# Kernel optimization log

Hardware: AMD Instinct MI355X
Metric: run time of the kernel (lower is better)

## Reference

```python
import jax, jax.numpy as jnp
import numpy as np
from jax import lax

DUNITS = 1024
ATT_DIM = 512
EPROJS = 512
ACONV_CHANS = 10
ACONV_FILTS = 100  # kernel size = 2*100+1 = 201
H_LEN = 16384
N_PREV = 128
SCALING = 2.0


def setup_inputs() -> dict:
    key = jax.random.key(0)
    ks = jax.random.split(key, 10)
    inv = lambda fan_in: 1.0 / np.sqrt(fan_in)
    return {
        "dec_z": jax.random.normal(ks[0], (1, DUNITS), jnp.float32),
        "att_prev": jax.random.uniform(ks[1], (N_PREV, 1, H_LEN), jnp.float32) / H_LEN,
        "pre_compute_enc_h": jax.random.normal(ks[2], (1, H_LEN, ATT_DIM), jnp.float32),
        "enc_h": jax.random.normal(ks[3], (1, H_LEN, EPROJS), jnp.float32),
        "mask": jnp.zeros((1, H_LEN), jnp.float32),
        # parameters (torch default inits, scale by 1/sqrt(fan_in))
        "loc_conv_w": jax.random.normal(ks[4], (ACONV_CHANS, 1, 2 * ACONV_FILTS + 1), jnp.float32) * inv(2 * ACONV_FILTS + 1),
        "mlp_att_w": jax.random.normal(ks[5], (ATT_DIM, ACONV_CHANS), jnp.float32) * inv(ACONV_CHANS),
        "mlp_dec_w": jax.random.normal(ks[6], (ATT_DIM, DUNITS), jnp.float32) * inv(DUNITS),
        "gvec_w": jax.random.normal(ks[7], (1, ATT_DIM), jnp.float32) * inv(ATT_DIM),
        "gvec_b": jnp.zeros((1,), jnp.float32),
    }


def reference(dec_z, att_prev, pre_compute_enc_h, enc_h, mask,
              loc_conv_w, mlp_att_w, mlp_dec_w, gvec_w, gvec_b):
    h_length = enc_h.shape[1]
    dec_z = dec_z.reshape(1, DUNITS)

    # coverage vector: sum of all previous attention distributions -> [1, h]
    cov_vec = jnp.sum(att_prev, axis=0)

    # location conv: Conv2d(1, C, (1, 2F+1)) on [1,1,1,h] == 1D conv on [1,1,h]
    att_conv = lax.conv_general_dilated(
        cov_vec[:, None, :], loc_conv_w,
        window_strides=(1,), padding=[(ACONV_FILTS, ACONV_FILTS)],
        dimension_numbers=("NCH", "OIH", "NCH"),
    )  # [1, C, h]
    # squeeze/transpose then mlp_att (no bias): [1, h, att_dim]
    att_conv = jnp.einsum("bch,ac->bha", att_conv, mlp_att_w)

    # mlp_dec (no bias), tiled over h: [1, 1, att_dim]
    dec_z_tiled = (dec_z @ mlp_dec_w.T)[:, None, :]

    # additive attention score e: [1, h]
    t = jnp.tanh(att_conv + pre_compute_enc_h + dec_z_tiled)
    e = jnp.einsum("bha,oa->bho", t, gvec_w)[..., 0] + gvec_b
    e = e + mask

    w = jax.nn.softmax(SCALING * e, axis=1)  # [1, h]

    att_prev_new = jnp.concatenate([att_prev, w[None]], axis=0)  # [n+1, 1, h]
    c = jnp.sum(enc_h * w[:, :, None], axis=1)  # [1, eprojs]
    return (c, att_prev_new)
```

## Files before the change

### kernel.cpp

```cpp
#include <hip/hip_runtime.h>

#define H_LEN 16384
#define ATT_DIM 512
#define DUNITS 1024
#define EPROJS 512
#define NCH 10
#define KFILT 201
#define PAD 100
#define N_PREV 128
#define HB 32
#define NB_SCORE 512
#define NB_FIN 256
#define NCOVP 16

__global__ __launch_bounds__(256) void k_prep(const float* __restrict__ att_prev,
                                              const float* __restrict__ mlp_dec_w,
                                              const float* __restrict__ dec_z,
                                              const float* __restrict__ watt,
                                              float* __restrict__ out_prev,
                                              float* __restrict__ cov16,
                                              float* __restrict__ dz,
                                              float* __restrict__ wattT,
                                              float* __restrict__ out_c) {
    int b = blockIdx.x, tid = threadIdx.x;
    if (b < 256) {
        const float4* ap4 = (const float4*)att_prev;
        float4* op4 = (float4*)out_prev;
        float4* cv4 = (float4*)cov16;
        int hb = b >> 4, q = b & 15;
        int idx0 = hb * 256 + tid;
        float4 s = {0.f, 0.f, 0.f, 0.f};
        #pragma unroll
        for (int n = q * 8; n < q * 8 + 8; ++n) {
            float4 v = ap4[n * (H_LEN / 4) + idx0];
            s.x += v.x; s.y += v.y; s.z += v.z; s.w += v.w;
            op4[n * (H_LEN / 4) + idx0] = v;
        }
        cv4[q * (H_LEN / 4) + idx0] = s;
    } else if (b < 384) {
        int lane = tid & 63;
        int a = (b - 256) * 4 + (tid >> 6);
        const float* row = mlp_dec_w + a * DUNITS;
        float s = 0.f;
        #pragma unroll
        for (int t = 0; t < DUNITS / 64; ++t) s += row[lane + 64 * t] * dec_z[lane + 64 * t];
        #pragma unroll
        for (int off = 32; off > 0; off >>= 1) s += __shfl_xor(s, off, 64);
        if (lane == 0) dz[a] = s;
    } else {
        out_c[tid] = 0.f;
        out_c[tid + 256] = 0.f;
        int a = tid * 2;
        #pragma unroll
        for (int c = 0; c < NCH; ++c) {
            wattT[c * ATT_DIM + a]     = watt[a * NCH + c];
            wattT[c * ATT_DIM + a + 1] = watt[(a + 1) * NCH + c];
        }
    }
}

__global__ __launch_bounds__(256, 2) void k_score(const float* __restrict__ cov16,
                                                  const float* __restrict__ cw,
                                                  const float* __restrict__ pre,
                                                  const float* __restrict__ mask,
                                                  const float* __restrict__ dz,
                                                  const float* __restrict__ wattT,
                                                  const float* __restrict__ gv,
                                                  const float* __restrict__ gb,
                                                  const float* __restrict__ enc,
                                                  float* __restrict__ vbuf,
                                                  float* __restrict__ pm,
                                                  float* __restrict__ ps,
                                                  float* __restrict__ pcb) {
    __shared__ float cov_s[HB + 2 * PAD];
    __shared__ float mask_s[HB];
    __shared__ float pc[8][NCH][HB];
    __shared__ float cfT[HB * 12];
    __shared__ float ew[4][HB];
    __shared__ float wt[HB];

    int tid = threadIdx.x, b = blockIdx.x;
    int h0 = b * HB;
    int lane = tid & 63, wv = tid >> 6;

    for (int i = tid; i < HB + 2 * PAD; i += 256) {
        int g = h0 - PAD + i;
        float s = 0.f;
        if (g >= 0 && g < H_LEN) {
            #pragma unroll
            for (int q = 0; q < NCOVP; ++q) s += cov16[q * H_LEN + g];
        }
        cov_s[i] = s;
    }
    if (tid < HB) mask_s[tid] = mask[h0 + tid];

    int a = (wv << 7) + (lane << 1);
    float2 dz2 = *(const float2*)(dz + a);
    float2 gv2 = *(const float2*)(gv + a);
    float W0[NCH], W1[NCH];
    #pragma unroll
    for (int c = 0; c < NCH; ++c) {
        float2 w = *(const float2*)(wattT + c * ATT_DIM + a);
        W0[c] = w.x; W1[c] = w.y;
    }
    float bias = gb[0];
    __syncthreads();

    {
        int h = tid & 31, q = tid >> 5;
        int k0 = (q * KFILT) / 8, k1 = ((q + 1) * KFILT) / 8;
        float acc[NCH];
        #pragma unroll
        for (int c = 0; c < NCH; ++c) acc[c] = 0.f;
        for (int k = k0; k < k1; ++k) {
            float s = cov_s[h + k];
            #pragma unroll
            for (int c = 0; c < NCH; ++c) acc[c] += s * cw[c * KFILT + k];
        }
        #pragma unroll
        for (int c = 0; c < NCH; ++c) pc[q][c][h] = acc[c];
    }
    __syncthreads();
    for (int i = tid; i < NCH * HB; i += 256) {
        int c = i >> 5, h = i & 31;
        float s = 0.f;
        #pragma unroll
        for (int q = 0; q < 8; ++q) s += pc[q][c][h];
        cfT[h * 12 + c] = s;
    }
    __syncthreads();

    float ea[HB];
    const float2* pre2 = (const float2*)pre;
    int colf2 = (wv << 6) + lane;
    #pragma unroll
    for (int hc = 0; hc < HB; hc += 8) {
        float2 Pr[8];
        #pragma unroll
        for (int j = 0; j < 8; ++j) Pr[j] = pre2[(h0 + hc + j) * 256 + colf2];
        #pragma unroll
        for (int j = 0; j < 8; ++j) {
            int h = hc + j;
            const float4* cp = (const float4*)&cfT[h * 12];
            float4 c0 = cp[0], c1 = cp[1], c2 = cp[2];
            float ch[NCH] = {c0.x, c0.y, c0.z, c0.w, c1.x, c1.y, c1.z, c1.w, c2.x, c2.y};
            float x0 = Pr[j].x + dz2.x;
            float x1 = Pr[j].y + dz2.y;
            #pragma unroll
            for (int c = 0; c < NCH; ++c) { x0 += ch[c] * W0[c]; x1 += ch[c] * W1[c]; }
            x0 = fminf(fmaxf(x0, -15.f), 15.f);
            x1 = fminf(fmaxf(x1, -15.f), 15.f);
            float z0 = __expf(2.f * x0), z1 = __expf(2.f * x1);
            float t0 = (z0 - 1.f) * __builtin_amdgcn_rcpf(z0 + 1.f);
            float t1 = (z1 - 1.f) * __builtin_amdgcn_rcpf(z1 + 1.f);
            ea[h] = t0 * gv2.x + t1 * gv2.y;
        }
    }

    #pragma unroll
    for (int k = 0; k < 16; ++k) {
        float up = __shfl_xor(ea[k + 16], 32, 64);
        float dn = __shfl_xor(ea[k], 32, 64);
        ea[k] = (lane & 32) ? (ea[k + 16] + up) : (ea[k] + dn);
    }
    #pragma unroll
    for (int k = 0; k < 8; ++k) {
        float up = __shfl_xor(ea[k + 8], 16, 64);
        float dn = __shfl_xor(ea[k], 16, 64);
        ea[k] = (lane & 16) ? (ea[k + 8] + up) : (ea[k] + dn);
    }
    #pragma unroll
    for (int k = 0; k < 4; ++k) {
        float up = __shfl_xor(ea[k + 4], 8, 64);
        float dn = __shfl_xor(ea[k], 8, 64);
        ea[k] = (lane & 8) ? (ea[k + 4] + up) : (ea[k] + dn);
    }
    #pragma unroll
    for (int k = 0; k < 2; ++k) {
        float up = __shfl_xor(ea[k + 2], 4, 64);
        float dn = __shfl_xor(ea[k], 4, 64);
        ea[k] = (lane & 4) ? (ea[k + 2] + up) : (ea[k] + dn);
    }
    {
        float up = __shfl_xor(ea[1], 2, 64);
        float dn = __shfl_xor(ea[0], 2, 64);
        ea[0] = (lane & 2) ? (ea[1] + up) : (ea[0] + dn);
    }
    ea[0] += __shfl_xor(ea[0], 1, 64);
    if ((lane & 1) == 0) ew[wv][lane >> 1] = ea[0];
    __syncthreads();

    if (wv == 0) {
        float v = -1e30f;
        if (lane < HB) {
            float e = ew[0][lane] + ew[1][lane] + ew[2][lane] + ew[3][lane];
            v = 2.f * (e + bias + mask_s[lane]);
            vbuf[h0 + lane] = v;
        }
        float m = v;
        #pragma unroll
        for (int off = 32; off > 0; off >>= 1) m = fmaxf(m, __shfl_xor(m, off, 64));
        float ev = (lane < HB) ? __expf(v - m) : 0.f;
        if (lane < HB) wt[lane] = ev;
        float s = ev;
        #pragma unroll
        for (int off = 32; off > 0; off >>= 1) s += __shfl_xor(s, off, 64);
        if (lane == 0) { pm[b] = m; ps[b] = s; }
    }
    __syncthreads();

    const float2* enc2 = (const float2*)enc;
    float2 acc0 = {0.f, 0.f}, acc1 = {0.f, 0.f};
    #pragma unroll
    for (int h = 0; h < HB; h += 2) {
        float w0 = wt[h], w1 = wt[h + 1];
        float2 e0 = enc2[(h0 + h) * 256 + tid];
        float2 e1 = enc2[(h0 + h + 1) * 256 + tid];
        acc0.x += w0 * e0.x; acc0.y += w0 * e0.y;
        acc1.x += w1 * e1.x; acc1.y += w1 * e1.y;
    }
    float2 accv = {acc0.x + acc1.x, acc0.y + acc1.y};
    ((float2*)pcb)[b * 256 + tid] = accv;
}

__global__ __launch_bounds__(256) void k_final(const float* __restrict__ vbuf,
                                               const float* __restrict__ pm,
                                               const float* __restrict__ ps,
                                               const float* __restrict__ pcb,
                                               float* __restrict__ out_w,
                                               float* __restrict__ out_c) {
    __shared__ float redA[4], redB[4];
    int tid = threadIdx.x, b = blockIdx.x;
    int lane = tid & 63, wv = tid >> 6;

    float m0 = pm[tid], m1 = pm[tid + 256];
    float s0 = ps[tid], s1 = ps[tid + 256];
    float m = fmaxf(m0, m1);
    #pragma unroll
    for (int off = 32; off > 0; off >>= 1) m = fmaxf(m, __shfl_xor(m, off, 64));
    if (lane == 0) redA[wv] = m;
    __syncthreads();
    float M = fmaxf(fmaxf(redA[0], redA[1]), fmaxf(redA[2], redA[3]));
    float s = s0 * __expf(m0 - M) + s1 * __expf(m1 - M);
    #pragma unroll
    for (int off = 32; off > 0; off >>= 1) s += __shfl_xor(s, off, 64);
    if (lane == 0) redB[wv] = s;
    __syncthreads();
    float S = redB[0] + redB[1] + redB[2] + redB[3];
    float rinv = 1.f / S;

    if (tid < 64) {
        int h = b * 64 + tid;
        out_w[h] = __expf(vbuf[h] - M) * rinv;
    }

    int r0 = 2 * b, r1 = 2 * b + 1;
    float sc0 = __expf(pm[r0] - M) * rinv;
    float sc1 = __expf(pm[r1] - M) * rinv;
    float v0 = pcb[r0 * EPROJS + tid] * sc0 + pcb[r1 * EPROJS + tid] * sc1;
    float v1 = pcb[r0 * EPROJS + tid + 256] * sc0 + pcb[r1 * EPROJS + tid + 256] * sc1;
    atomicAdd(&out_c[tid], v0);
    atomicAdd(&out_c[tid + 256], v1);
}

extern "C" void kernel_launch(void* const* d_in, const int* in_sizes, int n_in,
                              void* d_out, int out_size, void* d_ws, size_t ws_size,
                              hipStream_t stream) {
    const float* dec_z      = (const float*)d_in[0];
    const float* att_prev   = (const float*)d_in[1];
    const float* pre        = (const float*)d_in[2];
    const float* enc_h      = (const float*)d_in[3];
    const float* mask       = (const float*)d_in[4];
    const float* loc_conv_w = (const float*)d_in[5];
    const float* mlp_att_w  = (const float*)d_in[6];
    const float* mlp_dec_w  = (const float*)d_in[7];
    const float* gvec_w     = (const float*)d_in[8];
    const float* gvec_b     = (const float*)d_in[9];

    float* out_c    = (float*)d_out;
    float* out_prev = out_c + EPROJS;
    float* out_w    = out_prev + N_PREV * H_LEN;

    float* ws    = (float*)d_ws;
    float* cov16 = ws;
    float* dz    = cov16 + NCOVP * H_LEN;
    float* vb    = dz + ATT_DIM;
    float* pm    = vb + H_LEN;
    float* ps    = pm + NB_SCORE;
    float* pcb   = ps + NB_SCORE;
    float* wattT = pcb + NB_SCORE * EPROJS;

    k_prep<<<385, 256, 0, stream>>>(att_prev, mlp_dec_w, dec_z, mlp_att_w,
                                    out_prev, cov16, dz, wattT, out_c);
    k_score<<<NB_SCORE, 256, 0, stream>>>(cov16, loc_conv_w, pre, mask, dz, wattT,
                                          gvec_w, gvec_b, enc_h, vb, pm, ps, pcb);
    k_final<<<NB_FIN, 256, 0, stream>>>(vb, pm, ps, pcb, out_w, out_c);
}
```

Baseline: 139.2 us.

## Widen score kernel to 512 threads with one attention column per thread

The score kernel now runs 512 threads per block, each handling one attention/encoder column instead of two, with float2 loads replaced by scalar loads. The location-conv partial sums are split 16 ways and the score reduction runs across 8 waves. The butterfly shuffle reduction is rewritten to send a single value per stage instead of two. This aims to raise occupancy and latency hiding for the memory-bound pass, at the cost of narrower loads, more LDS partials and more cross-wave reduction.

```diff
diff --git a/kernel.cpp b/kernel.cpp
--- a/kernel.cpp
+++ b/kernel.cpp
@@ -59,7 +59,7 @@
     }
 }
 
-__global__ __launch_bounds__(256, 2) void k_score(const float* __restrict__ cov16,
+__global__ __launch_bounds__(512, 4) void k_score(const float* __restrict__ cov16,
                                                   const float* __restrict__ cw,
                                                   const float* __restrict__ pre,
                                                   const float* __restrict__ mask,
@@ -74,16 +74,16 @@
                                                   float* __restrict__ pcb) {
     __shared__ float cov_s[HB + 2 * PAD];
     __shared__ float mask_s[HB];
-    __shared__ float pc[8][NCH][HB];
+    __shared__ float pc[16][NCH][HB];
     __shared__ float cfT[HB * 12];
-    __shared__ float ew[4][HB];
+    __shared__ float ew[8][HB];
     __shared__ float wt[HB];
 
     int tid = threadIdx.x, b = blockIdx.x;
     int h0 = b * HB;
     int lane = tid & 63, wv = tid >> 6;
 
-    for (int i = tid; i < HB + 2 * PAD; i += 256) {
+    for (int i = tid; i < HB + 2 * PAD; i += 512) {
         int g = h0 - PAD + i;
         float s = 0.f;
         if (g >= 0 && g < H_LEN) {
@@ -94,21 +94,18 @@
     }
     if (tid < HB) mask_s[tid] = mask[h0 + tid];
 
-    int a = (wv << 7) + (lane << 1);
-    float2 dz2 = *(const float2*)(dz + a);
-    float2 gv2 = *(const float2*)(gv + a);
-    float W0[NCH], W1[NCH];
-    #pragma unroll
-    for (int c = 0; c < NCH; ++c) {
-        float2 w = *(const float2*)(wattT + c * ATT_DIM + a);
-        W0[c] = w.x; W1[c] = w.y;
-    }
+    int a = (wv << 6) + lane;
+    float dz1 = dz[a];
+    float gv1 = gv[a];
+    float W[NCH];
+    #pragma unroll
+    for (int c = 0; c < NCH; ++c) W[c] = wattT[c * ATT_DIM + a];
     float bias = gb[0];
     __syncthreads();
 
     {
         int h = tid & 31, q = tid >> 5;
-        int k0 = (q * KFILT) / 8, k1 = ((q + 1) * KFILT) / 8;
+        int k0 = (q * KFILT) / 16, k1 = ((q + 1) * KFILT) / 16;
         float acc[NCH];
         #pragma unroll
         for (int c = 0; c < NCH; ++c) acc[c] = 0.f;
@@ -121,70 +118,70 @@
         for (int c = 0; c < NCH; ++c) pc[q][c][h] = acc[c];
     }
     __syncthreads();
-    for (int i = tid; i < NCH * HB; i += 256) {
+    for (int i = tid; i < NCH * HB; i += 512) {
         int c = i >> 5, h = i & 31;
         float s = 0.f;
         #pragma unroll
-        for (int q = 0; q < 8; ++q) s += pc[q][c][h];
+        for (int q = 0; q < 16; ++q) s += pc[q][c][h];
         cfT[h * 12 + c] = s;
     }
     __syncthreads();
 
     float ea[HB];
-    const float2* pre2 = (const float2*)pre;
-    int colf2 = (wv << 6) + lane;
     #pragma unroll
     for (int hc = 0; hc < HB; hc += 8) {
-        float2 Pr[8];
-        #pragma unroll
-        for (int j = 0; j < 8; ++j) Pr[j] = pre2[(h0 + hc + j) * 256 + colf2];
+        float Pr[8];
+        #pragma unroll
+        for (int j = 0; j < 8; ++j) Pr[j] = pre[(h0 + hc + j) * ATT_DIM + a];
         #pragma unroll
         for (int j = 0; j < 8; ++j) {
             int h = hc + j;
             const float4* cp = (const float4*)&cfT[h * 12];
             float4 c0 = cp[0], c1 = cp[1], c2 = cp[2];
             float ch[NCH] = {c0.x, c0.y, c0.z, c0.w, c1.x, c1.y, c1.z, c1.w, c2.x, c2.y};
-            float x0 = Pr[j].x + dz2.x;
-            float x1 = Pr[j].y + dz2.y;
-            #pragma unroll
-            for (int c = 0; c < NCH; ++c) { x0 += ch[c] * W0[c]; x1 += ch[c] * W1[c]; }
-            x0 = fminf(fmaxf(x0, -15.f), 15.f);
-            x1 = fminf(fmaxf(x1, -15.f), 15.f);
-            float z0 = __expf(2.f * x0), z1 = __expf(2.f * x1);
-            float t0 = (z0 - 1.f) * __builtin_amdgcn_rcpf(z0 + 1.f);
-            float t1 = (z1 - 1.f) * __builtin_amdgcn_rcpf(z1 + 1.f);
-            ea[h] = t0 * gv2.x + t1 * gv2.y;
+            float x = Pr[j] + dz1;
+            #pragma unroll
+            for (int c = 0; c < NCH; ++c) x += ch[c] * W[c];
+            x = fminf(fmaxf(x, -15.f), 15.f);
+            float z = __expf(2.f * x);
+            float t = (z - 1.f) * __builtin_amdgcn_rcpf(z + 1.f);
+            ea[h] = t * gv1;
         }
     }
 
     #pragma unroll
     for (int k = 0; k < 16; ++k) {
-        float up = __shfl_xor(ea[k + 16], 32, 64);
-        float dn = __shfl_xor(ea[k], 32, 64);
-        ea[k] = (lane & 32) ? (ea[k + 16] + up) : (ea[k] + dn);
+        float lo = ea[k], hi = ea[k + 16];
+        float send = (lane & 32) ? lo : hi;
+        float recv = __shfl_xor(send, 32, 64);
+        ea[k] = ((lane & 32) ? hi : lo) + recv;
     }
     #pragma unroll
     for (int k = 0; k < 8; ++k) {
-        float up = __shfl_xor(ea[k + 8], 16, 64);
-        float dn = __shfl_xor(ea[k], 16, 64);
-        ea[k] = (lane & 16) ? (ea[k + 8] + up) : (ea[k] + dn);
+        float lo = ea[k], hi = ea[k + 8];
+        float send = (lane & 16) ? lo : hi;
+        float recv = __shfl_xor(send, 16, 64);
+        ea[k] = ((lane & 16) ? hi : lo) + recv;
     }
     #pragma unroll
     for (int k = 0; k < 4; ++k) {
-        float up = __shfl_xor(ea[k + 4], 8, 64);
-        float dn = __shfl_xor(ea[k], 8, 64);
-        ea[k] = (lane & 8) ? (ea[k + 4] + up) : (ea[k] + dn);
+        float lo = ea[k], hi = ea[k + 4];
+        float send = (lane & 8) ? lo : hi;
+        float recv = __shfl_xor(send, 8, 64);
+        ea[k] = ((lane & 8) ? hi : lo) + recv;
     }
     #pragma unroll
     for (int k = 0; k < 2; ++k) {
-        float up = __shfl_xor(ea[k + 2], 4, 64);
-        float dn = __shfl_xor(ea[k], 4, 64);
-        ea[k] = (lane & 4) ? (ea[k + 2] + up) : (ea[k] + dn);
+        float lo = ea[k], hi = ea[k + 2];
+        float send = (lane & 4) ? lo : hi;
+        float recv = __shfl_xor(send, 4, 64);
+        ea[k] = ((lane & 4) ? hi : lo) + recv;
     }
     {
-        float up = __shfl_xor(ea[1], 2, 64);
-        float dn = __shfl_xor(ea[0], 2, 64);
-        ea[0] = (lane & 2) ? (ea[1] + up) : (ea[0] + dn);
+        float lo = ea[0], hi = ea[1];
+        float send = (lane & 2) ? lo : hi;
+        float recv = __shfl_xor(send, 2, 64);
+        ea[0] = ((lane & 2) ? hi : lo) + recv;
     }
     ea[0] += __shfl_xor(ea[0], 1, 64);
     if ((lane & 1) == 0) ew[wv][lane >> 1] = ea[0];
@@ -193,7 +190,9 @@
     if (wv == 0) {
         float v = -1e30f;
         if (lane < HB) {
-            float e = ew[0][lane] + ew[1][lane] + ew[2][lane] + ew[3][lane];
+            float e = 0.f;
+            #pragma unroll
+            for (int w = 0; w < 8; ++w) e += ew[w][lane];
             v = 2.f * (e + bias + mask_s[lane]);
             vbuf[h0 + lane] = v;
         }
@@ -209,18 +208,13 @@
     }
     __syncthreads();
 
-    const float2* enc2 = (const float2*)enc;
-    float2 acc0 = {0.f, 0.f}, acc1 = {0.f, 0.f};
+    float ca0 = 0.f, ca1 = 0.f;
     #pragma unroll
     for (int h = 0; h < HB; h += 2) {
-        float w0 = wt[h], w1 = wt[h + 1];
-        float2 e0 = enc2[(h0 + h) * 256 + tid];
-        float2 e1 = enc2[(h0 + h + 1) * 256 + tid];
-        acc0.x += w0 * e0.x; acc0.y += w0 * e0.y;
-        acc1.x += w1 * e1.x; acc1.y += w1 * e1.y;
-    }
-    float2 accv = {acc0.x + acc1.x, acc0.y + acc1.y};
-    ((float2*)pcb)[b * 256 + tid] = accv;
+        ca0 += wt[h]     * enc[(h0 + h) * EPROJS + tid];
+        ca1 += wt[h + 1] * enc[(h0 + h + 1) * EPROJS + tid];
+    }
+    pcb[b * EPROJS + tid] = ca0 + ca1;
 }
 
 __global__ __launch_bounds__(256) void k_final(const float* __restrict__ vbuf,
@@ -292,7 +286,7 @@
 
     k_prep<<<385, 256, 0, stream>>>(att_prev, mlp_dec_w, dec_z, mlp_att_w,
                                     out_prev, cov16, dz, wattT, out_c);
-    k_score<<<NB_SCORE, 256, 0, stream>>>(cov16, loc_conv_w, pre, mask, dz, wattT,
+    k_score<<<NB_SCORE, 512, 0, stream>>>(cov16, loc_conv_w, pre, mask, dz, wattT,
                                           gvec_w, gvec_b, enc_h, vb, pm, ps, pcb);
     k_final<<<NB_FIN, 256, 0, stream>>>(vb, pm, ps, pcb, out_w, out_c);
 }
```

Result: slower. 145.9 us (+4.8%).

## Move att_prev copy into score kernel and halve shuffles in transpose-reduce

Applied to the files above, without the earlier changes.

The 8 MB copy of att_prev into the output is taken out of the prep kernel, which now only reads att_prev to build the coverage partials, and placed at the tail of each score block. Each of the 512 blocks copies 16 KB, so the copy shares the kernel with the compute-heavy scoring work, and prep becomes a read-only pass. The butterfly transpose-reduction now picks the value to send before the shuffle, so each stage issues one shuffle instead of two. The risk is that the score kernel carries extra memory traffic and register pressure, and att_prev is read twice from memory.

```diff
diff --git a/kernel.cpp b/kernel.cpp
--- a/kernel.cpp
+++ b/kernel.cpp
@@ -17,7 +17,6 @@
                                               const float* __restrict__ mlp_dec_w,
                                               const float* __restrict__ dec_z,
                                               const float* __restrict__ watt,
-                                              float* __restrict__ out_prev,
                                               float* __restrict__ cov16,
                                               float* __restrict__ dz,
                                               float* __restrict__ wattT,
@@ -25,7 +24,6 @@
     int b = blockIdx.x, tid = threadIdx.x;
     if (b < 256) {
         const float4* ap4 = (const float4*)att_prev;
-        float4* op4 = (float4*)out_prev;
         float4* cv4 = (float4*)cov16;
         int hb = b >> 4, q = b & 15;
         int idx0 = hb * 256 + tid;
@@ -34,7 +32,6 @@
         for (int n = q * 8; n < q * 8 + 8; ++n) {
             float4 v = ap4[n * (H_LEN / 4) + idx0];
             s.x += v.x; s.y += v.y; s.z += v.z; s.w += v.w;
-            op4[n * (H_LEN / 4) + idx0] = v;
         }
         cv4[q * (H_LEN / 4) + idx0] = s;
     } else if (b < 384) {
@@ -68,6 +65,8 @@
                                                   const float* __restrict__ gv,
                                                   const float* __restrict__ gb,
                                                   const float* __restrict__ enc,
+                                                  const float* __restrict__ att_prev,
+                                                  float* __restrict__ out_prev,
                                                   float* __restrict__ vbuf,
                                                   float* __restrict__ pm,
                                                   float* __restrict__ ps,
@@ -159,32 +158,37 @@
 
     #pragma unroll
     for (int k = 0; k < 16; ++k) {
-        float up = __shfl_xor(ea[k + 16], 32, 64);
-        float dn = __shfl_xor(ea[k], 32, 64);
-        ea[k] = (lane & 32) ? (ea[k + 16] + up) : (ea[k] + dn);
+        float lo = ea[k], hi = ea[k + 16];
+        float send = (lane & 32) ? lo : hi;
+        float recv = __shfl_xor(send, 32, 64);
+        ea[k] = ((lane & 32) ? hi : lo) + recv;
     }
     #pragma unroll
     for (int k = 0; k < 8; ++k) {
-        float up = __shfl_xor(ea[k + 8], 16, 64);
-        float dn = __shfl_xor(ea[k], 16, 64);
-        ea[k] = (lane & 16) ? (ea[k + 8] + up) : (ea[k] + dn);
+        float lo = ea[k], hi = ea[k + 8];
+        float send = (lane & 16) ? lo : hi;
+        float recv = __shfl_xor(send, 16, 64);
+        ea[k] = ((lane & 16) ? hi : lo) + recv;
     }
     #pragma unroll
     for (int k = 0; k < 4; ++k) {
-        float up = __shfl_xor(ea[k + 4], 8, 64);
-        float dn = __shfl_xor(ea[k], 8, 64);
-        ea[k] = (lane & 8) ? (ea[k + 4] + up) : (ea[k] + dn);
+        float lo = ea[k], hi = ea[k + 4];
+        float send = (lane & 8) ? lo : hi;
+        float recv = __shfl_xor(send, 8, 64);
+        ea[k] = ((lane & 8) ? hi : lo) + recv;
     }
     #pragma unroll
     for (int k = 0; k < 2; ++k) {
-        float up = __shfl_xor(ea[k + 2], 4, 64);
-        float dn = __shfl_xor(ea[k], 4, 64);
-        ea[k] = (lane & 4) ? (ea[k + 2] + up) : (ea[k] + dn);
+        float lo = ea[k], hi = ea[k + 2];
+        float send = (lane & 4) ? lo : hi;
+        float recv = __shfl_xor(send, 4, 64);
+        ea[k] = ((lane & 4) ? hi : lo) + recv;
     }
     {
-        float up = __shfl_xor(ea[1], 2, 64);
-        float dn = __shfl_xor(ea[0], 2, 64);
-        ea[0] = (lane & 2) ? (ea[1] + up) : (ea[0] + dn);
+        float lo = ea[0], hi = ea[1];
+        float send = (lane & 2) ? lo : hi;
+        float recv = __shfl_xor(send, 2, 64);
+        ea[0] = ((lane & 2) ? hi : lo) + recv;
     }
     ea[0] += __shfl_xor(ea[0], 1, 64);
     if ((lane & 1) == 0) ew[wv][lane >> 1] = ea[0];
@@ -221,6 +225,14 @@
     }
     float2 accv = {acc0.x + acc1.x, acc0.y + acc1.y};
     ((float2*)pcb)[b * 256 + tid] = accv;
+
+    {
+        const float4* ap4 = (const float4*)att_prev;
+        float4* op4 = (float4*)out_prev;
+        int ci = b * 1024 + tid;
+        #pragma unroll
+        for (int r = 0; r < 4; ++r) op4[ci + 256 * r] = ap4[ci + 256 * r];
+    }
 }
 
 __global__ __launch_bounds__(256) void k_final(const float* __restrict__ vbuf,
@@ -291,8 +303,9 @@
     float* wattT = pcb + NB_SCORE * EPROJS;
 
     k_prep<<<385, 256, 0, stream>>>(att_prev, mlp_dec_w, dec_z, mlp_att_w,
-                                    out_prev, cov16, dz, wattT, out_c);
+                                    cov16, dz, wattT, out_c);
     k_score<<<NB_SCORE, 256, 0, stream>>>(cov16, loc_conv_w, pre, mask, dz, wattT,
-                                          gvec_w, gvec_b, enc_h, vb, pm, ps, pcb);
+                                          gvec_w, gvec_b, enc_h, att_prev, out_prev,
+                                          vb, pm, ps, pcb);
     k_final<<<NB_FIN, 256, 0, stream>>>(vb, pm, ps, pcb, out_w, out_c);
 }
```

After: 140.4 us, median of 2. Within noise of the previous version (+0.9%).
